# Kernel tuning notes

Measured on AMD Instinct MI355X. Metric: run time of the kernel, lower is better.

The kernel has to match this reference:

```python
import jax, jax.numpy as jnp
import numpy as np

B, L, D, H = 8, 256, 512, 512
NEG_BIG = 1e8  # matches the 100000000.0 mask constant in the original


def setup_inputs() -> dict:
    key = jax.random.key(0)
    k1, k2, k3, k4 = jax.random.split(key, 4)
    enc = jax.random.normal(k1, (B, L, D), dtype=jnp.float32)
    # Glorot-uniform init, matching tf.keras.initializers.GlorotUniform
    s_w = float(np.sqrt(6.0 / (D + H)))
    W_l = jax.random.uniform(k2, (D, H), jnp.float32, -s_w, s_w)
    W_r = jax.random.uniform(k3, (D, H), jnp.float32, -s_w, s_w)
    s_u = float(np.sqrt(6.0 / (H + H)))  # 1-D glorot: fan_in = fan_out = H
    U = jax.random.uniform(k4, (H,), jnp.float32, -s_u, s_u)
    logit_bias = jnp.zeros((1,), jnp.float32)  # bias_initial_value=None -> zeros init
    return {"encoder_output": enc, "W_l": W_l, "W_r": W_r, "U": U, "logit_bias": logit_bias}


def reference(encoder_output, W_l, W_r, U, logit_bias):
    # dot_l[b,i,h], dot_r[b,j,h]
    dot_l = jnp.einsum('bik,kh->bih', encoder_output, W_l)
    dot_r = jnp.einsum('bjk,kh->bjh', encoder_output, W_r)
    # additive biaffine: tanh(dot_l_i + dot_r_j) . U  -> logits[b,i,j]
    final_sum = jnp.tanh(dot_l[:, :, None, :] + dot_r[:, None, :, :])  # [B,L,L,H]
    logits = jnp.einsum('bijh,h->bij', final_sum, U) + logit_bias[0]   # [B,L,L]
    # per-row self-mask (one_hot(i)) applied over all rows at once
    masked = logits - NEG_BIG * jnp.eye(L, dtype=logits.dtype)[None]   # [B,L,L]
    # original returns python lists over i of [B,L]; stack -> [L,B,L]
    mask_scores = jnp.transpose(masked, (1, 0, 2))
    p = jax.nn.sigmoid(mask_scores)
    samples = jax.random.bernoulli(jax.random.key(42), p).astype(jnp.int32)  # [L,B,L]
    # Bernoulli entropy from logits x: p*softplus(-x) + (1-p)*softplus(x)
    entropy = p * jax.nn.softplus(-mask_scores) + (1.0 - p) * jax.nn.softplus(mask_scores)
    return samples, mask_scores, entropy
```

## Files before the change

### kernel.cpp

```cpp
#include <hip/hip_runtime.h>
#include <stdint.h>

#define Bb 8
#define Ll 256
#define Dd 512
#define Hh 512
#define Nout (Ll * Bb * Ll)

#define Kc 2.8853900817779268

#define RNG_PARTITIONABLE 1

typedef __attribute__((ext_vector_type(8))) short bf16x8;
typedef __attribute__((ext_vector_type(4))) float f32x4;

__device__ __forceinline__ uint32_t rotl32(uint32_t v, int s) {
  return (v << s) | (v >> (32 - s));
}
__device__ __forceinline__ void tf_round(uint32_t& x0, uint32_t& x1, int r) {
  x0 += x1;
  x1 = rotl32(x1, r);
  x1 ^= x0;
}
__device__ __forceinline__ uint2 threefry2x32_k042(uint32_t x0, uint32_t x1) {
  const uint32_t k0 = 0u;
  const uint32_t k1 = 42u;
  const uint32_t k2 = 0x1BD11BDAu ^ k0 ^ k1;
  x0 += k0; x1 += k1;
  tf_round(x0, x1, 13); tf_round(x0, x1, 15); tf_round(x0, x1, 26); tf_round(x0, x1, 6);
  x0 += k1; x1 += k2 + 1u;
  tf_round(x0, x1, 17); tf_round(x0, x1, 29); tf_round(x0, x1, 16); tf_round(x0, x1, 24);
  x0 += k2; x1 += k0 + 2u;
  tf_round(x0, x1, 13); tf_round(x0, x1, 15); tf_round(x0, x1, 26); tf_round(x0, x1, 6);
  x0 += k0; x1 += k1 + 3u;
  tf_round(x0, x1, 17); tf_round(x0, x1, 29); tf_round(x0, x1, 16); tf_round(x0, x1, 24);
  x0 += k1; x1 += k2 + 4u;
  tf_round(x0, x1, 13); tf_round(x0, x1, 15); tf_round(x0, x1, 26); tf_round(x0, x1, 6);
  x0 += k2; x1 += k0 + 5u;
  return make_uint2(x0, x1);
}

__device__ __forceinline__ uint32_t rng_bits(uint32_t n) {
#if RNG_PARTITIONABLE
  uint2 o = threefry2x32_k042(0u, n);
  return o.x ^ o.y;
#else
  const uint32_t half = (uint32_t)(Nout / 2);
  if (n < half) {
    uint2 o = threefry2x32_k042(n, n + half);
    return o.x;
  } else {
    uint2 o = threefry2x32_k042(n - half, n);
    return o.y;
  }
#endif
}

__device__ __forceinline__ unsigned short bf16_rne(float f) {
  uint32_t u = __float_as_uint(f);
  u = (u + 0x7fffu + ((u >> 16) & 1u)) >> 16;
  return (unsigned short)u;
}
__device__ __forceinline__ float bf16_tof(unsigned short h) {
  return __uint_as_float(((uint32_t)h) << 16);
}
__device__ __forceinline__ void split3(float a, unsigned short& h,
                                       unsigned short& m, unsigned short& l) {
  h = bf16_rne(a);
  const float r1 = a - bf16_tof(h);
  m = bf16_rne(r1);
  const float r2 = r1 - bf16_tof(m);
  l = bf16_rne(r2);
}

__global__ __launch_bounds__(256) void split_enc(
    const float* __restrict__ enc, unsigned short* __restrict__ ah,
    unsigned short* __restrict__ am, unsigned short* __restrict__ al) {
  const int idx = (blockIdx.x * 256 + threadIdx.x) * 4;
  const float4 v = *(const float4*)(enc + idx);
  ushort4 h4, m4, l4;
  split3(v.x, h4.x, m4.x, l4.x);
  split3(v.y, h4.y, m4.y, l4.y);
  split3(v.z, h4.z, m4.z, l4.z);
  split3(v.w, h4.w, m4.w, l4.w);
  *(ushort4*)(ah + idx) = h4;
  *(ushort4*)(am + idx) = m4;
  *(ushort4*)(al + idx) = l4;
}

__global__ __launch_bounds__(256) void split_wt(
    const float* __restrict__ Wl, const float* __restrict__ Wr,
    unsigned short* __restrict__ wh, unsigned short* __restrict__ wm,
    unsigned short* __restrict__ wl) {
  const int z = blockIdx.z;
  const float* W = z ? Wr : Wl;
  const size_t zo = (size_t)z * Hh * Dd;
  const int k0 = blockIdx.x * 64;
  const int n0 = blockIdx.y * 64;
  __shared__ float tile[64][65];

  const int t = threadIdx.x;
#pragma unroll
  for (int rep = 0; rep < 4; ++rep) {
    const int idx = t + rep * 256;
    const int r = idx >> 4;
    const int c = (idx & 15) * 4;
    const float4 v = *(const float4*)(W + (size_t)(k0 + r) * Hh + n0 + c);
    tile[r][c + 0] = v.x; tile[r][c + 1] = v.y;
    tile[r][c + 2] = v.z; tile[r][c + 3] = v.w;
  }
  __syncthreads();
#pragma unroll
  for (int rep = 0; rep < 4; ++rep) {
    const int idx = t + rep * 256;
    const int rr = idx >> 4;
    const int cc = (idx & 15) * 4;
    ushort4 h4, m4, l4;
    split3(tile[cc + 0][rr], h4.x, m4.x, l4.x);
    split3(tile[cc + 1][rr], h4.y, m4.y, l4.y);
    split3(tile[cc + 2][rr], h4.z, m4.z, l4.z);
    split3(tile[cc + 3][rr], h4.w, m4.w, l4.w);
    const size_t o = zo + (size_t)(n0 + rr) * Dd + k0 + cc;
    *(ushort4*)(wh + o) = h4;
    *(ushort4*)(wm + o) = m4;
    *(ushort4*)(wl + o) = l4;
  }
}

__global__ __launch_bounds__(256) void gemm_mfma(
    const unsigned short* __restrict__ ah, const unsigned short* __restrict__ am,
    const unsigned short* __restrict__ al, const unsigned short* __restrict__ wh,
    const unsigned short* __restrict__ wm, const unsigned short* __restrict__ wl,
    float* __restrict__ el, float* __restrict__ er) {
  const int z = blockIdx.z;
  const size_t zo = (size_t)z * Hh * Dd;
  float* C = z ? er : el;
  const int m0 = blockIdx.x * 64;
  const int n0 = blockIdx.y * 64;

  __shared__ unsigned short Asm[2][12 * 512];
  __shared__ unsigned short Bsm[2][12 * 512];

  const int t = threadIdx.x;
  const int lane = t & 63;
  const int wv = t >> 6;
  const int l15 = lane & 15;
  const int kq8 = (lane >> 4) * 8;

  const unsigned short* gp[6];
  size_t go[6];
  int lq[6];
  bool isA[6];
#pragma unroll
  for (int s = 0; s < 6; ++s) {
    const int q = wv * 6 + s;
    if (q < 12) {
      const int p = q >> 2, mt = q & 3;
      gp[s] = (p == 0) ? ah : (p == 1) ? am : al;
      go[s] = (size_t)(m0 + mt * 16 + l15) * Dd + kq8;
      lq[s] = q * 512;
      isA[s] = true;
    } else {
      const int q2 = q - 12;
      const int p = q2 >> 2, nt = q2 & 3;
      gp[s] = (p == 0) ? wh : (p == 1) ? wm : wl;
      go[s] = zo + (size_t)(n0 + nt * 16 + l15) * Dd + kq8;
      lq[s] = q2 * 512;
      isA[s] = false;
    }
  }

  auto stage = [&](int buf, int kc) {
    const int k0 = kc * 32;
#pragma unroll
    for (int s = 0; s < 6; ++s) {
      unsigned short* dst = isA[s] ? &Asm[buf][lq[s]] : &Bsm[buf][lq[s]];
      __builtin_amdgcn_global_load_lds(
          (const __attribute__((address_space(1))) void*)(gp[s] + go[s] + k0),
          (__attribute__((address_space(3))) void*)dst, 16, 0, 0);
    }
  };

  const int mp = wv & 1;
  const int np = wv >> 1;

  f32x4 acc[2][2][2];
#pragma unroll
  for (int mi = 0; mi < 2; ++mi)
#pragma unroll
    for (int ni = 0; ni < 2; ++ni)
#pragma unroll
      for (int hf = 0; hf < 2; ++hf) acc[mi][ni][hf] = (f32x4){0.f, 0.f, 0.f, 0.f};

  stage(0, 0);
  __syncthreads();

  for (int kc = 0; kc < 16; ++kc) {
    const int buf = kc & 1;
    if (kc < 15) stage(buf ^ 1, kc + 1);

    bf16x8 af[2][3], bfr[2][3];
#pragma unroll
    for (int mi = 0; mi < 2; ++mi)
#pragma unroll
      for (int p = 0; p < 3; ++p)
        af[mi][p] = *(const bf16x8*)&Asm[buf][(p * 4 + mp * 2 + mi) * 512 + lane * 8];
#pragma unroll
    for (int ni = 0; ni < 2; ++ni)
#pragma unroll
      for (int p = 0; p < 3; ++p)
        bfr[ni][p] = *(const bf16x8*)&Bsm[buf][(p * 4 + np * 2 + ni) * 512 + lane * 8];

    const int hf = kc >> 3;
#pragma unroll
    for (int mi = 0; mi < 2; ++mi)
#pragma unroll
      for (int ni = 0; ni < 2; ++ni) {
        f32x4 A = acc[mi][ni][hf];
        A = __builtin_amdgcn_mfma_f32_16x16x32_bf16(af[mi][0], bfr[ni][0], A, 0, 0, 0);
        A = __builtin_amdgcn_mfma_f32_16x16x32_bf16(af[mi][0], bfr[ni][1], A, 0, 0, 0);
        A = __builtin_amdgcn_mfma_f32_16x16x32_bf16(af[mi][1], bfr[ni][0], A, 0, 0, 0);
        A = __builtin_amdgcn_mfma_f32_16x16x32_bf16(af[mi][0], bfr[ni][2], A, 0, 0, 0);
        A = __builtin_amdgcn_mfma_f32_16x16x32_bf16(af[mi][2], bfr[ni][0], A, 0, 0, 0);
        A = __builtin_amdgcn_mfma_f32_16x16x32_bf16(af[mi][1], bfr[ni][1], A, 0, 0, 0);
        acc[mi][ni][hf] = A;
      }
    __syncthreads();
  }

  const int rbase = (lane >> 4) * 4;
#pragma unroll
  for (int mi = 0; mi < 2; ++mi) {
    const int mbase = m0 + (mp * 2 + mi) * 16 + rbase;
#pragma unroll
    for (int ni = 0; ni < 2; ++ni) {
      const int n = n0 + (np * 2 + ni) * 16 + l15;
#pragma unroll
      for (int reg = 0; reg < 4; ++reg) {
        const double s = (double)acc[mi][ni][0][reg] + (double)acc[mi][ni][1][reg];
        C[(size_t)(mbase + reg) * Hh + n] = __builtin_amdgcn_exp2f((float)(Kc * s));
      }
    }
  }
}

__device__ __forceinline__ void group4_acc(float& S, const float4 a,
                                           const float4 bv, const float4 u) {
  const float d0 = __builtin_fmaf(a.x, bv.x, 1.0f);
  const float d1 = __builtin_fmaf(a.y, bv.y, 1.0f);
  const float d2 = __builtin_fmaf(a.z, bv.z, 1.0f);
  const float d3 = __builtin_fmaf(a.w, bv.w, 1.0f);
  const float p01 = d0 * d1;
  const float p23 = d2 * d3;
  const float D = p01 * p23;
  float n01 = u.x * d1;
  n01 = __builtin_fmaf(u.y, d0, n01);
  float n23 = u.z * d3;
  n23 = __builtin_fmaf(u.w, d2, n23);
  float num = n01 * p23;
  num = __builtin_fmaf(n23, p01, num);
  S = __builtin_fmaf(num, __builtin_amdgcn_rcpf(D), S);
}

__global__ __launch_bounds__(256) void biaffine_part(
    const float* __restrict__ el, const float* __restrict__ er,
    const float* __restrict__ U, float* __restrict__ part) {
  const int zz = blockIdx.z;
  const int b = zz & 7;
  const int ks = zz >> 3;
  const int i0 = blockIdx.y * 64;
  const int j0 = blockIdx.x * 64;
  const int h0 = ks * 64;

  __shared__ float els[64][68];
  __shared__ float ers[64][68];
  __shared__ float us[64];

  const int t = threadIdx.x;
  if (t < 16) *(float4*)&us[t * 4] = *(const float4*)(U + h0 + t * 4);

  const float* elg = el + (size_t)(b * Ll + i0) * Hh + h0;
  const float* erg = er + (size_t)(b * Ll + j0) * Hh + h0;
#pragma unroll
  for (int rep = 0; rep < 4; ++rep) {
    const int idx = t + rep * 256;
    const int r = idx >> 4;
    const int c = (idx & 15) * 4;
    *(float4*)&els[r][c] = *(const float4*)(elg + (size_t)r * Hh + c);
    *(float4*)&ers[r][c] = *(const float4*)(erg + (size_t)r * Hh + c);
  }
  __syncthreads();

  float usl = 0.0f;
#pragma unroll
  for (int q = 0; q < 16; ++q) {
    const float4 u = *(const float4*)&us[q * 4];
    usl += ((u.x + u.y) + u.z) + u.w;
  }

  const int ti = t >> 4;
  const int tj = t & 15;

  float S[4][4];
#pragma unroll
  for (int r = 0; r < 4; ++r)
#pragma unroll
    for (int c = 0; c < 4; ++c) S[r][c] = 0.0f;

  for (int g = 0; g < 16; ++g) {
    const int h = g * 4;
    const float4 u = *(const float4*)&us[h];
    float4 av[4], bv[4];
#pragma unroll
    for (int c = 0; c < 4; ++c) {
      av[c] = *(const float4*)&els[ti + 16 * c][h];
      bv[c] = *(const float4*)&ers[tj + 16 * c][h];
    }
#pragma unroll
    for (int r = 0; r < 4; ++r)
#pragma unroll
      for (int c = 0; c < 4; ++c) group4_acc(S[r][c], av[r], bv[c], u);
  }

  float* pslice = part + (size_t)ks * Nout;
#pragma unroll
  for (int r = 0; r < 4; ++r) {
    const int i = i0 + ti + 16 * r;
#pragma unroll
    for (int c = 0; c < 4; ++c) {
      const int j = j0 + tj + 16 * c;
      const uint32_t n = ((uint32_t)i * Bb + (uint32_t)b) * Ll + (uint32_t)j;
      pslice[n] = __builtin_fmaf(-2.0f, S[r][c], usl);
    }
  }
}

__global__ __launch_bounds__(256) void biaffine_emit(
    const float* __restrict__ part, const float* __restrict__ biasp,
    float* __restrict__ out) {
  const uint32_t n4 = (blockIdx.x * 256u + threadIdx.x) * 4u;
  double s0 = 0.0, s1 = 0.0, s2 = 0.0, s3 = 0.0;
#pragma unroll
  for (int k = 0; k < 8; ++k) {
    const float4 v = *(const float4*)(part + (size_t)k * Nout + n4);
    s0 += (double)v.x;
    s1 += (double)v.y;
    s2 += (double)v.z;
    s3 += (double)v.w;
  }
  const float bias = biasp[0];
  const double sv[4] = {s0, s1, s2, s3};

  float4 samp4, x4, ent4;
  float* sp = &samp4.x;
  float* xp = &x4.x;
  float* ep = &ent4.x;
#pragma unroll
  for (int q = 0; q < 4; ++q) {
    const uint32_t n = n4 + q;
    const int i = (int)(n >> 11);
    const int j = (int)(n & 255u);
    float x = (float)sv[q] + bias;
    if (i == j) x -= 1e8f;

    const double pd = 1.0 / (1.0 + exp(-(double)x));
    const float pf = (float)pd;

    const uint32_t bits = rng_bits(n);
    const float uu = __uint_as_float((bits >> 9) | 0x3f800000u) - 1.0f;
    sp[q] = (uu < pf) ? 1.0f : 0.0f;
    xp[q] = x;

    const float ax = fabsf(x);
    const float l1p = log1pf(expf(-ax));
    const float sp_pos = fmaxf(x, 0.0f) + l1p;
    const float sp_neg = fmaxf(-x, 0.0f) + l1p;
    ep[q] = pf * sp_neg + (1.0f - pf) * sp_pos;
  }
  *(float4*)(out + n4) = samp4;
  *(float4*)(out + Nout + n4) = x4;
  *(float4*)(out + 2 * (size_t)Nout + n4) = ent4;
}

extern "C" void kernel_launch(void* const* d_in, const int* in_sizes, int n_in,
                              void* d_out, int out_size, void* d_ws,
                              size_t ws_size, hipStream_t stream) {
  const float* enc = (const float*)d_in[0];
  const float* Wl = (const float*)d_in[1];
  const float* Wr = (const float*)d_in[2];
  const float* U = (const float*)d_in[3];
  const float* lb = (const float*)d_in[4];
  float* out = (float*)d_out;

  char* w = (char*)d_ws;
  float* el = (float*)w;                      w += (size_t)Bb * Ll * Hh * 4;
  float* er = (float*)w;                      w += (size_t)Bb * Ll * Hh * 4;
  float* part = (float*)w;                    w += (size_t)8 * Nout * 4;
  unsigned short* ah = (unsigned short*)w;    w += (size_t)Bb * Ll * Dd * 2;
  unsigned short* am = (unsigned short*)w;    w += (size_t)Bb * Ll * Dd * 2;
  unsigned short* al = (unsigned short*)w;    w += (size_t)Bb * Ll * Dd * 2;
  unsigned short* wh = (unsigned short*)w;    w += (size_t)2 * Dd * Hh * 2;
  unsigned short* wm = (unsigned short*)w;    w += (size_t)2 * Dd * Hh * 2;
  unsigned short* wl = (unsigned short*)w;    w += (size_t)2 * Dd * Hh * 2;

  split_enc<<<dim3((Bb * Ll * Dd) / 1024), 256, 0, stream>>>(enc, ah, am, al);
  split_wt<<<dim3(Dd / 64, Hh / 64, 2), 256, 0, stream>>>(Wl, Wr, wh, wm, wl);
  gemm_mfma<<<dim3((Bb * Ll) / 64, Hh / 64, 2), 256, 0, stream>>>(
      ah, am, al, wh, wm, wl, el, er);
  biaffine_part<<<dim3(Ll / 64, Ll / 64, Bb * 8), 256, 0, stream>>>(el, er, U, part);
  biaffine_emit<<<dim3(Nout / 1024), 256, 0, stream>>>(part, lb, out);
}
```

Baseline: 127.2 us.

## Halve GEMM N-tile and double biaffine H-split for more blocks

The projection GEMM now uses 64x32 output tiles, doubling grid size, and each wave computes one 16-row strip with a reworked load assignment. The biaffine partial kernel splits the hidden dimension into 16 chunks of 32 instead of 8 of 64, doubling block count, and the emit kernel sums 16 partial slices. This raises parallelism and occupancy on the large GPU, at the cost of doubling partial-sum memory traffic and workspace, and reducing per-block reuse in the GEMM.

```diff
diff --git a/kernel.cpp b/kernel.cpp
--- a/kernel.cpp
+++ b/kernel.cpp
@@ -8,6 +8,7 @@
 #define Nout (Ll * Bb * Ll)
 
 #define Kc 2.8853900817779268
+#define KSPLIT 16
 
 #define RNG_PARTITIONABLE 1
 
@@ -136,10 +137,10 @@
   const size_t zo = (size_t)z * Hh * Dd;
   float* C = z ? er : el;
   const int m0 = blockIdx.x * 64;
-  const int n0 = blockIdx.y * 64;
+  const int n0 = blockIdx.y * 32;
 
   __shared__ unsigned short Asm[2][12 * 512];
-  __shared__ unsigned short Bsm[2][12 * 512];
+  __shared__ unsigned short Bsm[2][6 * 512];
 
   const int t = threadIdx.x;
   const int lane = t & 63;
@@ -147,33 +148,35 @@
   const int l15 = lane & 15;
   const int kq8 = (lane >> 4) * 8;
 
-  const unsigned short* gp[6];
-  size_t go[6];
-  int lq[6];
-  bool isA[6];
-#pragma unroll
-  for (int s = 0; s < 6; ++s) {
-    const int q = wv * 6 + s;
+  const unsigned short* gp[5];
+  size_t go[5];
+  int lq[5];
+  bool isA[5];
+  int nld = 0;
+#pragma unroll
+  for (int s = 0; s < 5; ++s) {
+    const int q = s * 4 + wv;
     if (q < 12) {
       const int p = q >> 2, mt = q & 3;
-      gp[s] = (p == 0) ? ah : (p == 1) ? am : al;
-      go[s] = (size_t)(m0 + mt * 16 + l15) * Dd + kq8;
-      lq[s] = q * 512;
-      isA[s] = true;
-    } else {
+      gp[nld] = (p == 0) ? ah : (p == 1) ? am : al;
+      go[nld] = (size_t)(m0 + mt * 16 + l15) * Dd + kq8;
+      lq[nld] = q * 512;
+      isA[nld] = true;
+      ++nld;
+    } else if (q < 18) {
       const int q2 = q - 12;
-      const int p = q2 >> 2, nt = q2 & 3;
-      gp[s] = (p == 0) ? wh : (p == 1) ? wm : wl;
-      go[s] = zo + (size_t)(n0 + nt * 16 + l15) * Dd + kq8;
-      lq[s] = q2 * 512;
-      isA[s] = false;
+      const int p = q2 >> 1, nt = q2 & 1;
+      gp[nld] = (p == 0) ? wh : (p == 1) ? wm : wl;
+      go[nld] = zo + (size_t)(n0 + nt * 16 + l15) * Dd + kq8;
+      lq[nld] = q2 * 512;
+      isA[nld] = false;
+      ++nld;
     }
   }
 
   auto stage = [&](int buf, int kc) {
     const int k0 = kc * 32;
-#pragma unroll
-    for (int s = 0; s < 6; ++s) {
+    for (int s = 0; s < nld; ++s) {
       unsigned short* dst = isA[s] ? &Asm[buf][lq[s]] : &Bsm[buf][lq[s]];
       __builtin_amdgcn_global_load_lds(
           (const __attribute__((address_space(1))) void*)(gp[s] + go[s] + k0),
@@ -181,16 +184,11 @@
     }
   };
 
-  const int mp = wv & 1;
-  const int np = wv >> 1;
-
-  f32x4 acc[2][2][2];
-#pragma unroll
-  for (int mi = 0; mi < 2; ++mi)
-#pragma unroll
-    for (int ni = 0; ni < 2; ++ni)
-#pragma unroll
-      for (int hf = 0; hf < 2; ++hf) acc[mi][ni][hf] = (f32x4){0.f, 0.f, 0.f, 0.f};
+  f32x4 acc[2][2];
+#pragma unroll
+  for (int ni = 0; ni < 2; ++ni)
+#pragma unroll
+    for (int hf = 0; hf < 2; ++hf) acc[ni][hf] = (f32x4){0.f, 0.f, 0.f, 0.f};
 
   stage(0, 0);
   __syncthreads();
@@ -199,47 +197,40 @@
     const int buf = kc & 1;
     if (kc < 15) stage(buf ^ 1, kc + 1);
 
-    bf16x8 af[2][3], bfr[2][3];
-#pragma unroll
-    for (int mi = 0; mi < 2; ++mi)
+    bf16x8 af[3], bfr[2][3];
+#pragma unroll
+    for (int p = 0; p < 3; ++p)
+      af[p] = *(const bf16x8*)&Asm[buf][(p * 4 + wv) * 512 + lane * 8];
+#pragma unroll
+    for (int ni = 0; ni < 2; ++ni)
 #pragma unroll
       for (int p = 0; p < 3; ++p)
-        af[mi][p] = *(const bf16x8*)&Asm[buf][(p * 4 + mp * 2 + mi) * 512 + lane * 8];
-#pragma unroll
-    for (int ni = 0; ni < 2; ++ni)
-#pragma unroll
-      for (int p = 0; p < 3; ++p)
-        bfr[ni][p] = *(const bf16x8*)&Bsm[buf][(p * 4 + np * 2 + ni) * 512 + lane * 8];
+        bfr[ni][p] = *(const bf16x8*)&Bsm[buf][(p * 2 + ni) * 512 + lane * 8];
 
     const int hf = kc >> 3;
 #pragma unroll
-    for (int mi = 0; mi < 2; ++mi)
-#pragma unroll
-      for (int ni = 0; ni < 2; ++ni) {
-        f32x4 A = acc[mi][ni][hf];
-        A = __builtin_amdgcn_mfma_f32_16x16x32_bf16(af[mi][0], bfr[ni][0], A, 0, 0, 0);
-        A = __builtin_amdgcn_mfma_f32_16x16x32_bf16(af[mi][0], bfr[ni][1], A, 0, 0, 0);
-        A = __builtin_amdgcn_mfma_f32_16x16x32_bf16(af[mi][1], bfr[ni][0], A, 0, 0, 0);
-        A = __builtin_amdgcn_mfma_f32_16x16x32_bf16(af[mi][0], bfr[ni][2], A, 0, 0, 0);
-        A = __builtin_amdgcn_mfma_f32_16x16x32_bf16(af[mi][2], bfr[ni][0], A, 0, 0, 0);
-        A = __builtin_amdgcn_mfma_f32_16x16x32_bf16(af[mi][1], bfr[ni][1], A, 0, 0, 0);
-        acc[mi][ni][hf] = A;
-      }
+    for (int ni = 0; ni < 2; ++ni) {
+      f32x4 A = acc[ni][hf];
+      A = __builtin_amdgcn_mfma_f32_16x16x32_bf16(af[0], bfr[ni][0], A, 0, 0, 0);
+      A = __builtin_amdgcn_mfma_f32_16x16x32_bf16(af[0], bfr[ni][1], A, 0, 0, 0);
+      A = __builtin_amdgcn_mfma_f32_16x16x32_bf16(af[1], bfr[ni][0], A, 0, 0, 0);
+      A = __builtin_amdgcn_mfma_f32_16x16x32_bf16(af[0], bfr[ni][2], A, 0, 0, 0);
+      A = __builtin_amdgcn_mfma_f32_16x16x32_bf16(af[2], bfr[ni][0], A, 0, 0, 0);
+      A = __builtin_amdgcn_mfma_f32_16x16x32_bf16(af[1], bfr[ni][1], A, 0, 0, 0);
+      acc[ni][hf] = A;
+    }
     __syncthreads();
   }
 
   const int rbase = (lane >> 4) * 4;
-#pragma unroll
-  for (int mi = 0; mi < 2; ++mi) {
-    const int mbase = m0 + (mp * 2 + mi) * 16 + rbase;
-#pragma unroll
-    for (int ni = 0; ni < 2; ++ni) {
-      const int n = n0 + (np * 2 + ni) * 16 + l15;
-#pragma unroll
-      for (int reg = 0; reg < 4; ++reg) {
-        const double s = (double)acc[mi][ni][0][reg] + (double)acc[mi][ni][1][reg];
-        C[(size_t)(mbase + reg) * Hh + n] = __builtin_amdgcn_exp2f((float)(Kc * s));
-      }
+  const int mbase = m0 + wv * 16 + rbase;
+#pragma unroll
+  for (int ni = 0; ni < 2; ++ni) {
+    const int n = n0 + ni * 16 + l15;
+#pragma unroll
+    for (int reg = 0; reg < 4; ++reg) {
+      const double s = (double)acc[ni][0][reg] + (double)acc[ni][1][reg];
+      C[(size_t)(mbase + reg) * Hh + n] = __builtin_amdgcn_exp2f((float)(Kc * s));
     }
   }
 }
@@ -270,22 +261,22 @@
   const int ks = zz >> 3;
   const int i0 = blockIdx.y * 64;
   const int j0 = blockIdx.x * 64;
-  const int h0 = ks * 64;
-
-  __shared__ float els[64][68];
-  __shared__ float ers[64][68];
-  __shared__ float us[64];
+  const int h0 = ks * 32;
+
+  __shared__ float els[64][36];
+  __shared__ float ers[64][36];
+  __shared__ float us[32];
 
   const int t = threadIdx.x;
-  if (t < 16) *(float4*)&us[t * 4] = *(const float4*)(U + h0 + t * 4);
+  if (t < 8) *(float4*)&us[t * 4] = *(const float4*)(U + h0 + t * 4);
 
   const float* elg = el + (size_t)(b * Ll + i0) * Hh + h0;
   const float* erg = er + (size_t)(b * Ll + j0) * Hh + h0;
 #pragma unroll
-  for (int rep = 0; rep < 4; ++rep) {
+  for (int rep = 0; rep < 2; ++rep) {
     const int idx = t + rep * 256;
-    const int r = idx >> 4;
-    const int c = (idx & 15) * 4;
+    const int r = idx >> 3;
+    const int c = (idx & 7) * 4;
     *(float4*)&els[r][c] = *(const float4*)(elg + (size_t)r * Hh + c);
     *(float4*)&ers[r][c] = *(const float4*)(erg + (size_t)r * Hh + c);
   }
@@ -293,7 +284,7 @@
 
   float usl = 0.0f;
 #pragma unroll
-  for (int q = 0; q < 16; ++q) {
+  for (int q = 0; q < 8; ++q) {
     const float4 u = *(const float4*)&us[q * 4];
     usl += ((u.x + u.y) + u.z) + u.w;
   }
@@ -307,7 +298,8 @@
 #pragma unroll
     for (int c = 0; c < 4; ++c) S[r][c] = 0.0f;
 
-  for (int g = 0; g < 16; ++g) {
+#pragma unroll
+  for (int g = 0; g < 8; ++g) {
     const int h = g * 4;
     const float4 u = *(const float4*)&us[h];
     float4 av[4], bv[4];
@@ -341,7 +333,7 @@
   const uint32_t n4 = (blockIdx.x * 256u + threadIdx.x) * 4u;
   double s0 = 0.0, s1 = 0.0, s2 = 0.0, s3 = 0.0;
 #pragma unroll
-  for (int k = 0; k < 8; ++k) {
+  for (int k = 0; k < KSPLIT; ++k) {
     const float4 v = *(const float4*)(part + (size_t)k * Nout + n4);
     s0 += (double)v.x;
     s1 += (double)v.y;
@@ -395,7 +387,7 @@
   char* w = (char*)d_ws;
   float* el = (float*)w;                      w += (size_t)Bb * Ll * Hh * 4;
   float* er = (float*)w;                      w += (size_t)Bb * Ll * Hh * 4;
-  float* part = (float*)w;                    w += (size_t)8 * Nout * 4;
+  float* part = (float*)w;                    w += (size_t)KSPLIT * Nout * 4;
   unsigned short* ah = (unsigned short*)w;    w += (size_t)Bb * Ll * Dd * 2;
   unsigned short* am = (unsigned short*)w;    w += (size_t)Bb * Ll * Dd * 2;
   unsigned short* al = (unsigned short*)w;    w += (size_t)Bb * Ll * Dd * 2;
@@ -405,8 +397,9 @@
 
   split_enc<<<dim3((Bb * Ll * Dd) / 1024), 256, 0, stream>>>(enc, ah, am, al);
   split_wt<<<dim3(Dd / 64, Hh / 64, 2), 256, 0, stream>>>(Wl, Wr, wh, wm, wl);
-  gemm_mfma<<<dim3((Bb * Ll) / 64, Hh / 64, 2), 256, 0, stream>>>(
+  gemm_mfma<<<dim3((Bb * Ll) / 64, Hh / 32, 2), 256, 0, stream>>>(
       ah, am, al, wh, wm, wl, el, er);
-  biaffine_part<<<dim3(Ll / 64, Ll / 64, Bb * 8), 256, 0, stream>>>(el, er, U, part);
+  biaffine_part<<<dim3(Ll / 64, Ll / 64, Bb * KSPLIT), 256, 0, stream>>>(
+      el, er, U, part);
   biaffine_emit<<<dim3(Nout / 1024), 256, 0, stream>>>(part, lb, out);
 }
```

Measured after the change: 203.3 us. +59.8%, slower.

## Split GEMM K across blocks, move exp into biaffine, enlarge biaffine tiles

Applied to the files above, without the earlier changes.

The projection GEMM now splits its K dimension into two halves run as separate blocks (grid z=4) without double buffering, writing raw partial sums. The exp2 conversion moves into the biaffine kernel's load stage, where it sums the two partials. The biaffine kernel uses 128x128 tiles with an 8x8 per-thread register block over a 32-wide H slice, so the K-split count rises to 16 partial buffers. The aim is more GEMM parallelism and more register reuse in the dominant tanh-sum stage, at the cost of more partial-sum memory traffic, a larger emit reduction, single-buffered GEMM loads and higher register pressure.

```diff
diff --git a/kernel.cpp b/kernel.cpp
--- a/kernel.cpp
+++ b/kernel.cpp
@@ -8,6 +8,8 @@
 #define Nout (Ll * Bb * Ll)
 
 #define Kc 2.8853900817779268
+#define KSPLIT 16
+#define HS ((size_t)2048 * 512)
 
 #define RNG_PARTITIONABLE 1
 
@@ -131,15 +133,17 @@
     const unsigned short* __restrict__ ah, const unsigned short* __restrict__ am,
     const unsigned short* __restrict__ al, const unsigned short* __restrict__ wh,
     const unsigned short* __restrict__ wm, const unsigned short* __restrict__ wl,
-    float* __restrict__ el, float* __restrict__ er) {
+    float* __restrict__ dh) {
   const int z = blockIdx.z;
-  const size_t zo = (size_t)z * Hh * Dd;
-  float* C = z ? er : el;
+  const int zW = z & 1;
+  const int half = z >> 1;
+  const size_t zo = (size_t)zW * Hh * Dd;
+  float* out = dh + ((size_t)zW * 2 + half) * HS;
   const int m0 = blockIdx.x * 64;
   const int n0 = blockIdx.y * 64;
 
-  __shared__ unsigned short Asm[2][12 * 512];
-  __shared__ unsigned short Bsm[2][12 * 512];
+  __shared__ unsigned short Asm[12 * 512];
+  __shared__ unsigned short Bsm[12 * 512];
 
   const int t = threadIdx.x;
   const int lane = t & 63;
@@ -170,60 +174,51 @@
     }
   }
 
-  auto stage = [&](int buf, int kc) {
-    const int k0 = kc * 32;
+  const int mp = wv & 1;
+  const int np = wv >> 1;
+
+  f32x4 acc[2][2];
+#pragma unroll
+  for (int mi = 0; mi < 2; ++mi)
+#pragma unroll
+    for (int ni = 0; ni < 2; ++ni) acc[mi][ni] = (f32x4){0.f, 0.f, 0.f, 0.f};
+
+  const int kbase = half * 8;
+  for (int kc2 = 0; kc2 < 8; ++kc2) {
+    const int k0 = (kbase + kc2) * 32;
 #pragma unroll
     for (int s = 0; s < 6; ++s) {
-      unsigned short* dst = isA[s] ? &Asm[buf][lq[s]] : &Bsm[buf][lq[s]];
+      unsigned short* dst = isA[s] ? &Asm[lq[s]] : &Bsm[lq[s]];
       __builtin_amdgcn_global_load_lds(
           (const __attribute__((address_space(1))) void*)(gp[s] + go[s] + k0),
           (__attribute__((address_space(3))) void*)dst, 16, 0, 0);
     }
-  };
-
-  const int mp = wv & 1;
-  const int np = wv >> 1;
-
-  f32x4 acc[2][2][2];
-#pragma unroll
-  for (int mi = 0; mi < 2; ++mi)
+    __syncthreads();
+
+    bf16x8 af[2][3], bfr[2][3];
+#pragma unroll
+    for (int mi = 0; mi < 2; ++mi)
+#pragma unroll
+      for (int p = 0; p < 3; ++p)
+        af[mi][p] = *(const bf16x8*)&Asm[(p * 4 + mp * 2 + mi) * 512 + lane * 8];
 #pragma unroll
     for (int ni = 0; ni < 2; ++ni)
 #pragma unroll
-      for (int hf = 0; hf < 2; ++hf) acc[mi][ni][hf] = (f32x4){0.f, 0.f, 0.f, 0.f};
-
-  stage(0, 0);
-  __syncthreads();
-
-  for (int kc = 0; kc < 16; ++kc) {
-    const int buf = kc & 1;
-    if (kc < 15) stage(buf ^ 1, kc + 1);
-
-    bf16x8 af[2][3], bfr[2][3];
+      for (int p = 0; p < 3; ++p)
+        bfr[ni][p] = *(const bf16x8*)&Bsm[(p * 4 + np * 2 + ni) * 512 + lane * 8];
+
 #pragma unroll
     for (int mi = 0; mi < 2; ++mi)
 #pragma unroll
-      for (int p = 0; p < 3; ++p)
-        af[mi][p] = *(const bf16x8*)&Asm[buf][(p * 4 + mp * 2 + mi) * 512 + lane * 8];
-#pragma unroll
-    for (int ni = 0; ni < 2; ++ni)
-#pragma unroll
-      for (int p = 0; p < 3; ++p)
-        bfr[ni][p] = *(const bf16x8*)&Bsm[buf][(p * 4 + np * 2 + ni) * 512 + lane * 8];
-
-    const int hf = kc >> 3;
-#pragma unroll
-    for (int mi = 0; mi < 2; ++mi)
-#pragma unroll
       for (int ni = 0; ni < 2; ++ni) {
-        f32x4 A = acc[mi][ni][hf];
+        f32x4 A = acc[mi][ni];
         A = __builtin_amdgcn_mfma_f32_16x16x32_bf16(af[mi][0], bfr[ni][0], A, 0, 0, 0);
         A = __builtin_amdgcn_mfma_f32_16x16x32_bf16(af[mi][0], bfr[ni][1], A, 0, 0, 0);
         A = __builtin_amdgcn_mfma_f32_16x16x32_bf16(af[mi][1], bfr[ni][0], A, 0, 0, 0);
         A = __builtin_amdgcn_mfma_f32_16x16x32_bf16(af[mi][0], bfr[ni][2], A, 0, 0, 0);
         A = __builtin_amdgcn_mfma_f32_16x16x32_bf16(af[mi][2], bfr[ni][0], A, 0, 0, 0);
         A = __builtin_amdgcn_mfma_f32_16x16x32_bf16(af[mi][1], bfr[ni][1], A, 0, 0, 0);
-        acc[mi][ni][hf] = A;
+        acc[mi][ni] = A;
       }
     __syncthreads();
   }
@@ -236,10 +231,8 @@
     for (int ni = 0; ni < 2; ++ni) {
       const int n = n0 + (np * 2 + ni) * 16 + l15;
 #pragma unroll
-      for (int reg = 0; reg < 4; ++reg) {
-        const double s = (double)acc[mi][ni][0][reg] + (double)acc[mi][ni][1][reg];
-        C[(size_t)(mbase + reg) * Hh + n] = __builtin_amdgcn_exp2f((float)(Kc * s));
-      }
+      for (int reg = 0; reg < 4; ++reg)
+        out[(size_t)(mbase + reg) * Hh + n] = acc[mi][ni][reg];
     }
   }
 }
@@ -263,71 +256,92 @@
 }
 
 __global__ __launch_bounds__(256) void biaffine_part(
-    const float* __restrict__ el, const float* __restrict__ er,
-    const float* __restrict__ U, float* __restrict__ part) {
+    const float* __restrict__ dh, const float* __restrict__ U,
+    float* __restrict__ part) {
   const int zz = blockIdx.z;
   const int b = zz & 7;
   const int ks = zz >> 3;
-  const int i0 = blockIdx.y * 64;
-  const int j0 = blockIdx.x * 64;
-  const int h0 = ks * 64;
-
-  __shared__ float els[64][68];
-  __shared__ float ers[64][68];
-  __shared__ float us[64];
+  const int i0 = blockIdx.y * 128;
+  const int j0 = blockIdx.x * 128;
+  const int h0s = ks * 32;
+
+  __shared__ float els[128][36];
+  __shared__ float ers[128][36];
 
   const int t = threadIdx.x;
-  if (t < 16) *(float4*)&us[t * 4] = *(const float4*)(U + h0 + t * 4);
-
-  const float* elg = el + (size_t)(b * Ll + i0) * Hh + h0;
-  const float* erg = er + (size_t)(b * Ll + j0) * Hh + h0;
+
+  const float* el0 = dh + 0 * HS;
+  const float* el1 = dh + 1 * HS;
+  const float* er0 = dh + 2 * HS;
+  const float* er1 = dh + 3 * HS;
+
 #pragma unroll
   for (int rep = 0; rep < 4; ++rep) {
     const int idx = t + rep * 256;
-    const int r = idx >> 4;
-    const int c = (idx & 15) * 4;
-    *(float4*)&els[r][c] = *(const float4*)(elg + (size_t)r * Hh + c);
-    *(float4*)&ers[r][c] = *(const float4*)(erg + (size_t)r * Hh + c);
+    const int r = idx >> 3;
+    const int c = (idx & 7) * 4;
+    {
+      const size_t off = (size_t)(b * Ll + i0 + r) * Hh + h0s + c;
+      const float4 a0 = *(const float4*)(el0 + off);
+      const float4 a1 = *(const float4*)(el1 + off);
+      float4 e;
+      e.x = __builtin_amdgcn_exp2f((float)(Kc * ((double)a0.x + (double)a1.x)));
+      e.y = __builtin_amdgcn_exp2f((float)(Kc * ((double)a0.y + (double)a1.y)));
+      e.z = __builtin_amdgcn_exp2f((float)(Kc * ((double)a0.z + (double)a1.z)));
+      e.w = __builtin_amdgcn_exp2f((float)(Kc * ((double)a0.w + (double)a1.w)));
+      *(float4*)&els[r][c] = e;
+    }
+    {
+      const size_t off = (size_t)(b * Ll + j0 + r) * Hh + h0s + c;
+      const float4 a0 = *(const float4*)(er0 + off);
+      const float4 a1 = *(const float4*)(er1 + off);
+      float4 e;
+      e.x = __builtin_amdgcn_exp2f((float)(Kc * ((double)a0.x + (double)a1.x)));
+      e.y = __builtin_amdgcn_exp2f((float)(Kc * ((double)a0.y + (double)a1.y)));
+      e.z = __builtin_amdgcn_exp2f((float)(Kc * ((double)a0.z + (double)a1.z)));
+      e.w = __builtin_amdgcn_exp2f((float)(Kc * ((double)a0.w + (double)a1.w)));
+      *(float4*)&ers[r][c] = e;
+    }
   }
   __syncthreads();
 
   float usl = 0.0f;
 #pragma unroll
-  for (int q = 0; q < 16; ++q) {
-    const float4 u = *(const float4*)&us[q * 4];
+  for (int q = 0; q < 8; ++q) {
+    const float4 u = *(const float4*)(U + h0s + q * 4);
     usl += ((u.x + u.y) + u.z) + u.w;
   }
 
   const int ti = t >> 4;
   const int tj = t & 15;
 
-  float S[4][4];
-#pragma unroll
-  for (int r = 0; r < 4; ++r)
-#pragma unroll
-    for (int c = 0; c < 4; ++c) S[r][c] = 0.0f;
-
-  for (int g = 0; g < 16; ++g) {
+  float S[8][8];
+#pragma unroll
+  for (int r = 0; r < 8; ++r)
+#pragma unroll
+    for (int c = 0; c < 8; ++c) S[r][c] = 0.0f;
+
+  for (int g = 0; g < 8; ++g) {
     const int h = g * 4;
-    const float4 u = *(const float4*)&us[h];
-    float4 av[4], bv[4];
-#pragma unroll
-    for (int c = 0; c < 4; ++c) {
+    const float4 u = *(const float4*)(U + h0s + h);
+    float4 av[8], bv[8];
+#pragma unroll
+    for (int c = 0; c < 8; ++c) {
       av[c] = *(const float4*)&els[ti + 16 * c][h];
       bv[c] = *(const float4*)&ers[tj + 16 * c][h];
     }
 #pragma unroll
-    for (int r = 0; r < 4; ++r)
-#pragma unroll
-      for (int c = 0; c < 4; ++c) group4_acc(S[r][c], av[r], bv[c], u);
+    for (int r = 0; r < 8; ++r)
+#pragma unroll
+      for (int c = 0; c < 8; ++c) group4_acc(S[r][c], av[r], bv[c], u);
   }
 
   float* pslice = part + (size_t)ks * Nout;
 #pragma unroll
-  for (int r = 0; r < 4; ++r) {
+  for (int r = 0; r < 8; ++r) {
     const int i = i0 + ti + 16 * r;
 #pragma unroll
-    for (int c = 0; c < 4; ++c) {
+    for (int c = 0; c < 8; ++c) {
       const int j = j0 + tj + 16 * c;
       const uint32_t n = ((uint32_t)i * Bb + (uint32_t)b) * Ll + (uint32_t)j;
       pslice[n] = __builtin_fmaf(-2.0f, S[r][c], usl);
@@ -341,7 +355,7 @@
   const uint32_t n4 = (blockIdx.x * 256u + threadIdx.x) * 4u;
   double s0 = 0.0, s1 = 0.0, s2 = 0.0, s3 = 0.0;
 #pragma unroll
-  for (int k = 0; k < 8; ++k) {
+  for (int k = 0; k < KSPLIT; ++k) {
     const float4 v = *(const float4*)(part + (size_t)k * Nout + n4);
     s0 += (double)v.x;
     s1 += (double)v.y;
@@ -393,9 +407,8 @@
   float* out = (float*)d_out;
 
   char* w = (char*)d_ws;
-  float* el = (float*)w;                      w += (size_t)Bb * Ll * Hh * 4;
-  float* er = (float*)w;                      w += (size_t)Bb * Ll * Hh * 4;
-  float* part = (float*)w;                    w += (size_t)8 * Nout * 4;
+  float* dh = (float*)w;                      w += 4 * HS * 4;
+  float* part = (float*)w;                    w += (size_t)KSPLIT * Nout * 4;
   unsigned short* ah = (unsigned short*)w;    w += (size_t)Bb * Ll * Dd * 2;
   unsigned short* am = (unsigned short*)w;    w += (size_t)Bb * Ll * Dd * 2;
   unsigned short* al = (unsigned short*)w;    w += (size_t)Bb * Ll * Dd * 2;
@@ -405,8 +418,9 @@
 
   split_enc<<<dim3((Bb * Ll * Dd) / 1024), 256, 0, stream>>>(enc, ah, am, al);
   split_wt<<<dim3(Dd / 64, Hh / 64, 2), 256, 0, stream>>>(Wl, Wr, wh, wm, wl);
-  gemm_mfma<<<dim3((Bb * Ll) / 64, Hh / 64, 2), 256, 0, stream>>>(
-      ah, am, al, wh, wm, wl, el, er);
-  biaffine_part<<<dim3(Ll / 64, Ll / 64, Bb * 8), 256, 0, stream>>>(el, er, U, part);
+  gemm_mfma<<<dim3((Bb * Ll) / 64, Hh / 64, 4), 256, 0, stream>>>(
+      ah, am, al, wh, wm, wl, dh);
+  biaffine_part<<<dim3(Ll / 128, Ll / 128, Bb * KSPLIT), 256, 0, stream>>>(
+      dh, U, part);
   biaffine_emit<<<dim3(Nout / 1024), 256, 0, stream>>>(part, lb, out);
 }
```

After: 131.8 us. 3.6% more time.
